# Kernel optimization log

Hardware: AMD Instinct MI355X
Metric: run time of the kernel (lower is better)

The kernel has to match this reference:

```python
import jax, jax.numpy as jnp
import numpy as np

B, H, N, HD = 8, 12, 577, 64   # batch, heads, tokens (576 patches + CLS), head dim
GRID = 24                      # 384 / 16
TEMP = 0.1                     # RelaxedBernoulli temperature
EPS = 1e-6


def _make_dists():
    # pairwise (row,col) offsets between patch grid positions, CLS row/col padded with 0
    r, c = np.indices((GRID, GRID))
    idx = np.stack([r.ravel(), c.ravel()], axis=-1).astype(np.float32)   # (576, 2)
    d = idx[:, None, :] - idx[None, :, :]                                # (576, 576, 2)
    d = np.pad(d, ((1, 0), (1, 0), (0, 0)))                              # (577, 577, 2)
    return jnp.asarray(d)


def setup_inputs() -> dict:
    key = jax.random.key(0)
    kq, k1, k2, ku = jax.random.split(key, 4)
    return {
        "query": jax.random.normal(kq, (B, H, N, HD), dtype=jnp.float32),
        "W1": jax.random.normal(k1, (HD, 64), dtype=jnp.float32) * 0.02,
        "b1": jnp.zeros((64,), dtype=jnp.float32),
        "W2": jax.random.normal(k2, (64, 3), dtype=jnp.float32) * 0.02,
        "b2": jnp.zeros((3,), dtype=jnp.float32),
        "u": jax.random.uniform(ku, (B, H, N, N), dtype=jnp.float32,
                                minval=EPS, maxval=1.0 - EPS),
        "dists": _make_dists(),
    }


def reference(query, W1, b1, W2, b2, u, dists):
    # sigma MLP: Linear -> gelu -> Linear  ->  (b,h,n,3)
    s = jax.nn.gelu(query @ W1 + b1, approximate=False) @ W2 + b2

    # per-token 2x2 covariance: [[sx^2, rho*sx*sy], [rho*sx*sy, sy^2]]
    sx = jax.nn.relu(s[..., 0]) + 1.0
    sy = jax.nn.relu(s[..., 1]) + 1.0
    rho = 0.99 * jnp.tanh(s[..., 2])
    sxx = sx * sx
    syy = sy * sy
    sxy = rho * sx * sy

    # closed-form 2x2 inverse
    det = sxx * syy - sxy * sxy
    inv00 = syy / det
    inv11 = sxx / det
    inv01 = -sxy / det

    # quadratic form d^T Sinv d without materializing (b,h,n,n,2,2)
    dx = dists[..., 0]   # (n, n)
    dy = dists[..., 1]
    w = -0.5 * (jnp.einsum('bhi,ij->bhij', inv00, dx * dx)
                + 2.0 * jnp.einsum('bhi,ij->bhij', inv01, dx * dy)
                + jnp.einsum('bhi,ij->bhij', inv11, dy * dy))

    kernel = jnp.exp(w)
    probs = kernel / jnp.max(kernel, axis=-1, keepdims=True)
    probs = jnp.clip(probs, EPS, 1.0 - EPS)

    # RelaxedBernoulli reparameterized sample with logistic noise from u
    logits = jnp.log(probs) - jnp.log1p(-probs)
    noise = jnp.log(u) - jnp.log1p(-u)
    mask = jax.nn.sigmoid((logits + noise) / TEMP)
    return mask
```

## Files before the change

### kernel.cpp

```cpp
#include <hip/hip_runtime.h>
#include <math.h>

#define BHN     55392
#define NTOK    577
#define HD      64
#define EPS_F   1e-6f
#define TOTAL_ELEMS 31961184
#define TOTAL_VEC   7990296

__global__ __launch_bounds__(256) void sigma_coef_kernel(
    const float* __restrict__ q,  const float* __restrict__ W1,
    const float* __restrict__ b1, const float* __restrict__ W2,
    const float* __restrict__ b2, float4* __restrict__ coef)
{
    const int tok = blockIdx.x * 256 + threadIdx.x;
    if (tok >= BHN) return;

    float h[HD];
    #pragma unroll
    for (int t = 0; t < HD; ++t) h[t] = 0.0f;

    const float4* w1_4 = (const float4*)W1;
    const float4* q4   = (const float4*)(q + (size_t)tok * HD);
    float4 qv = q4[0];
    #pragma unroll 1
    for (int kk = 0; kk < 16; ++kk) {
        const int kn = (kk < 15) ? (kk + 1) : 15;
        float4 qnext = q4[kn];
        float qk[4] = {qv.x, qv.y, qv.z, qv.w};
        #pragma unroll
        for (int d = 0; d < 4; ++d) {
            float qs = qk[d];
            const int base = (kk * 4 + d) * 16;
            #pragma unroll
            for (int t4 = 0; t4 < 16; ++t4) {
                float4 wv = w1_4[base + t4];
                h[4*t4+0] = fmaf(qs, wv.x, h[4*t4+0]);
                h[4*t4+1] = fmaf(qs, wv.y, h[4*t4+1]);
                h[4*t4+2] = fmaf(qs, wv.z, h[4*t4+2]);
                h[4*t4+3] = fmaf(qs, wv.w, h[4*t4+3]);
            }
        }
        qv = qnext;
    }

    float s0 = b2[0], s1 = b2[1], s2 = b2[2];
    #pragma unroll
    for (int t = 0; t < HD; ++t) {
        float x = h[t] + b1[t];
        float z = x * 0.70710678118654752f;
        float az = fabsf(z);
        float k = __builtin_amdgcn_rcpf(fmaf(0.3275911f, az, 1.0f));
        float poly = k * (0.254829592f + k * (-0.284496736f +
                     k * (1.421413741f + k * (-1.453152027f +
                     k * 1.061405429f))));
        float om = poly * __expf(-z * z);
        float erfz = copysignf(1.0f - om, z);
        float g = 0.5f * x * (1.0f + erfz);
        s0 = fmaf(g, W2[t*3 + 0], s0);
        s1 = fmaf(g, W2[t*3 + 1], s1);
        s2 = fmaf(g, W2[t*3 + 2], s2);
    }

    float sx = fmaxf(s0, 0.0f) + 1.0f;
    float sy = fmaxf(s1, 0.0f) + 1.0f;
    float ex = __expf(2.0f * s2);
    float rho = 0.99f * ((ex - 1.0f) * __builtin_amdgcn_rcpf(ex + 1.0f));
    float sxx = sx * sx, syy = sy * sy;
    float sxy = rho * sx * sy;
    float det = sxx * syy - sxy * sxy;
    float inv_det = 1.0f / det;

    float a = -0.5f * syy * inv_det;
    float b =  sxy * inv_det;
    float c = -0.5f * sxx * inv_det;

    int i = tok % NTOK;
    float pack;
    if (i == 0) { a = 0.0f; b = 0.0f; c = 0.0f; pack = 0.0f; }
    else {
        int ip = i - 1;
        int ri = ip / 24;
        int ci = ip - ri * 24;
        pack = (float)(ri * 32 + ci);
    }
    coef[tok] = make_float4(a, b, c, pack);
}

__global__ __launch_bounds__(256) void mask_kernel(
    const float4* __restrict__ u4, const float4* __restrict__ coef,
    float4* __restrict__ out4)
{
    int vid = blockIdx.x * 256 + threadIdx.x;
    if (vid >= TOTAL_VEC) return;

    int e0 = vid * 4;
    unsigned row0 = (unsigned)e0 / 577u;
    int j0 = e0 - (int)row0 * 577;

    unsigned row1 = row0 + ((j0 + 3 >= 577) ? 1u : 0u);
    float4 cf0 = coef[row0];
    float4 cf1 = coef[row1];
    float4 uu = u4[vid];

    float um[4] = {uu.x, uu.y, uu.z, uu.w};
    float res[4];

    #pragma unroll
    for (int m = 0; m < 4; ++m) {
        int j = j0 + m;
        bool crossed = (j >= 577);
        if (crossed) j -= 577;
        float4 cf;
        cf.x = crossed ? cf1.x : cf0.x;
        cf.y = crossed ? cf1.y : cf0.y;
        cf.z = crossed ? cf1.z : cf0.z;
        cf.w = crossed ? cf1.w : cf0.w;
        int rc = (int)cf.w;

        float dx = 0.0f, dy = 0.0f;
        if (j > 0) {
            unsigned jj = (unsigned)(j - 1);
            unsigned rj = jj / 24u;
            unsigned cj = jj - rj * 24u;
            dx = (float)((rc >> 5) - (int)rj);
            dy = (float)((rc & 31) - (int)cj);
        }

        float w = fmaf(fmaf(cf.x, dx, cf.y * dy), dx, cf.z * (dy * dy));

        float p = __expf(w);
        p = fminf(fmaxf(p, EPS_F), 1.0f - EPS_F);

        float uk  = um[m];
        float num = p * uk;
        float den = (1.0f - p) * (1.0f - uk);
        float r   = den * __builtin_amdgcn_rcpf(num);

        float r2  = r * r;
        float r4  = r2 * r2;
        float r5  = r4 * r;
        float r10 = r5 * r5;

        res[m] = __builtin_amdgcn_rcpf(1.0f + r10);
    }

    out4[vid] = make_float4(res[0], res[1], res[2], res[3]);
}

extern "C" void kernel_launch(void* const* d_in, const int* in_sizes, int n_in,
                              void* d_out, int out_size, void* d_ws, size_t ws_size,
                              hipStream_t stream) {
    const float* q  = (const float*)d_in[0];
    const float* W1 = (const float*)d_in[1];
    const float* b1 = (const float*)d_in[2];
    const float* W2 = (const float*)d_in[3];
    const float* b2 = (const float*)d_in[4];
    const float* u  = (const float*)d_in[5];

    float4* coef = (float4*)d_ws;

    sigma_coef_kernel<<<(BHN + 255) / 256, 256, 0, stream>>>(q, W1, b1, W2, b2, coef);
    mask_kernel<<<(TOTAL_VEC + 255) / 256, 256, 0, stream>>>(
        (const float4*)u, coef, (float4*)d_out);
}
```

Baseline: 266.6 us.

## Split sigma MLP hidden dimension across 8 lanes per token with shuffle reduction

The sigma MLP kernel now assigns 8 threads per token, each computing 8 of the 64 hidden units, and combines the three output partial sums with xor-shuffles. This cuts per-thread register use (64 accumulators down to 8) and launches 8x more threads, which should raise occupancy and parallelism for the small first kernel. In exchange, each lane reloads the full query row, the reduction adds shuffles, and only one lane in eight does the final covariance math and store. The mask kernel, which likely dominates the total time, is unchanged.

```diff
diff --git a/kernel.cpp b/kernel.cpp
--- a/kernel.cpp
+++ b/kernel.cpp
@@ -13,15 +13,19 @@
     const float* __restrict__ b1, const float* __restrict__ W2,
     const float* __restrict__ b2, float4* __restrict__ coef)
 {
-    const int tok = blockIdx.x * 256 + threadIdx.x;
+    const int tid   = threadIdx.x;
+    const int slice = tid & 7;
+    const int tok   = blockIdx.x * 32 + (tid >> 3);
     if (tok >= BHN) return;
 
-    float h[HD];
+    float h[8];
     #pragma unroll
-    for (int t = 0; t < HD; ++t) h[t] = 0.0f;
+    for (int t = 0; t < 8; ++t) h[t] = 0.0f;
 
-    const float4* w1_4 = (const float4*)W1;
-    const float4* q4   = (const float4*)(q + (size_t)tok * HD);
+    const float4* q4    = (const float4*)(q + (size_t)tok * HD);
+    const float4* w1_4  = (const float4*)W1;
+    const int     woff  = slice * 2;
+
     float4 qv = q4[0];
     #pragma unroll 1
     for (int kk = 0; kk < 16; ++kk) {
@@ -30,24 +34,27 @@
         float qk[4] = {qv.x, qv.y, qv.z, qv.w};
         #pragma unroll
         for (int d = 0; d < 4; ++d) {
+            const float4* wrow = w1_4 + (kk * 4 + d) * 16 + woff;
+            float4 w0 = wrow[0];
+            float4 w1v = wrow[1];
             float qs = qk[d];
-            const int base = (kk * 4 + d) * 16;
-            #pragma unroll
-            for (int t4 = 0; t4 < 16; ++t4) {
-                float4 wv = w1_4[base + t4];
-                h[4*t4+0] = fmaf(qs, wv.x, h[4*t4+0]);
-                h[4*t4+1] = fmaf(qs, wv.y, h[4*t4+1]);
-                h[4*t4+2] = fmaf(qs, wv.z, h[4*t4+2]);
-                h[4*t4+3] = fmaf(qs, wv.w, h[4*t4+3]);
-            }
+            h[0] = fmaf(qs, w0.x, h[0]);
+            h[1] = fmaf(qs, w0.y, h[1]);
+            h[2] = fmaf(qs, w0.z, h[2]);
+            h[3] = fmaf(qs, w0.w, h[3]);
+            h[4] = fmaf(qs, w1v.x, h[4]);
+            h[5] = fmaf(qs, w1v.y, h[5]);
+            h[6] = fmaf(qs, w1v.z, h[6]);
+            h[7] = fmaf(qs, w1v.w, h[7]);
         }
         qv = qnext;
     }
 
-    float s0 = b2[0], s1 = b2[1], s2 = b2[2];
+    float s0 = 0.0f, s1 = 0.0f, s2 = 0.0f;
+    const int tbase = slice * 8;
     #pragma unroll
-    for (int t = 0; t < HD; ++t) {
-        float x = h[t] + b1[t];
+    for (int t = 0; t < 8; ++t) {
+        float x = h[t] + b1[tbase + t];
         float z = x * 0.70710678118654752f;
         float az = fabsf(z);
         float k = __builtin_amdgcn_rcpf(fmaf(0.3275911f, az, 1.0f));
@@ -57,34 +64,41 @@
         float om = poly * __expf(-z * z);
         float erfz = copysignf(1.0f - om, z);
         float g = 0.5f * x * (1.0f + erfz);
-        s0 = fmaf(g, W2[t*3 + 0], s0);
-        s1 = fmaf(g, W2[t*3 + 1], s1);
-        s2 = fmaf(g, W2[t*3 + 2], s2);
+        s0 = fmaf(g, W2[(tbase + t)*3 + 0], s0);
+        s1 = fmaf(g, W2[(tbase + t)*3 + 1], s1);
+        s2 = fmaf(g, W2[(tbase + t)*3 + 2], s2);
     }
 
-    float sx = fmaxf(s0, 0.0f) + 1.0f;
-    float sy = fmaxf(s1, 0.0f) + 1.0f;
-    float ex = __expf(2.0f * s2);
-    float rho = 0.99f * ((ex - 1.0f) * __builtin_amdgcn_rcpf(ex + 1.0f));
-    float sxx = sx * sx, syy = sy * sy;
-    float sxy = rho * sx * sy;
-    float det = sxx * syy - sxy * sxy;
-    float inv_det = 1.0f / det;
+    s0 += __shfl_xor(s0, 1); s0 += __shfl_xor(s0, 2); s0 += __shfl_xor(s0, 4);
+    s1 += __shfl_xor(s1, 1); s1 += __shfl_xor(s1, 2); s1 += __shfl_xor(s1, 4);
+    s2 += __shfl_xor(s2, 1); s2 += __shfl_xor(s2, 2); s2 += __shfl_xor(s2, 4);
 
-    float a = -0.5f * syy * inv_det;
-    float b =  sxy * inv_det;
-    float c = -0.5f * sxx * inv_det;
+    if (slice == 0) {
+        s0 += b2[0]; s1 += b2[1]; s2 += b2[2];
+        float sx = fmaxf(s0, 0.0f) + 1.0f;
+        float sy = fmaxf(s1, 0.0f) + 1.0f;
+        float ex = __expf(2.0f * s2);
+        float rho = 0.99f * ((ex - 1.0f) * __builtin_amdgcn_rcpf(ex + 1.0f));
+        float sxx = sx * sx, syy = sy * sy;
+        float sxy = rho * sx * sy;
+        float det = sxx * syy - sxy * sxy;
+        float inv_det = 1.0f / det;
 
-    int i = tok % NTOK;
-    float pack;
-    if (i == 0) { a = 0.0f; b = 0.0f; c = 0.0f; pack = 0.0f; }
-    else {
-        int ip = i - 1;
-        int ri = ip / 24;
-        int ci = ip - ri * 24;
-        pack = (float)(ri * 32 + ci);
+        float a = -0.5f * syy * inv_det;
+        float b =  sxy * inv_det;
+        float c = -0.5f * sxx * inv_det;
+
+        int i = tok % NTOK;
+        float pack;
+        if (i == 0) { a = 0.0f; b = 0.0f; c = 0.0f; pack = 0.0f; }
+        else {
+            int ip = i - 1;
+            int ri = ip / 24;
+            int ci = ip - ri * 24;
+            pack = (float)(ri * 32 + ci);
+        }
+        coef[tok] = make_float4(a, b, c, pack);
     }
-    coef[tok] = make_float4(a, b, c, pack);
 }
 
 __global__ __launch_bounds__(256) void mask_kernel(
@@ -160,7 +174,7 @@
 
     float4* coef = (float4*)d_ws;
 
-    sigma_coef_kernel<<<(BHN + 255) / 256, 256, 0, stream>>>(q, W1, b1, W2, b2, coef);
+    sigma_coef_kernel<<<(BHN + 31) / 32, 256, 0, stream>>>(q, W1, b1, W2, b2, coef);
     mask_kernel<<<(TOTAL_VEC + 255) / 256, 256, 0, stream>>>(
         (const float4*)u, coef, (float4*)d_out);
 }
```

Measured after the change: 267.7 us. No clear change (+0.4%).

## Fuse sigma MLP into mask kernel with per-wave row MLP and nontemporal IO

Applied to the files above, without the earlier changes.

Merges the two launches into one kernel. Each block handles 4 rows: each wavefront computes one token's MLP with lanes over the hidden dimension and a shuffle reduction, then writes the coefficients to shared memory. The block then streams the 4 rows of u to output with nontemporal loads and stores. This removes the second launch and the coefficient round trip through global memory, at the cost of a per-block MLP phase and a barrier before streaming. It also leaves only about 577 vectors per 256-thread block, so some threads sit idle in the second loop iteration.

```diff
diff --git a/kernel.cpp b/kernel.cpp
--- a/kernel.cpp
+++ b/kernel.cpp
@@ -1,151 +1,139 @@
 #include <hip/hip_runtime.h>
 #include <math.h>
 
-#define BHN     55392
-#define NTOK    577
-#define HD      64
-#define EPS_F   1e-6f
-#define TOTAL_ELEMS 31961184
-#define TOTAL_VEC   7990296
+#define BHN    55392
+#define NTOK   577
+#define HD     64
+#define EPS_F  1e-6f
+#define ROWS_PER_BLOCK 4
+#define NBLOCKS (BHN / ROWS_PER_BLOCK)
+#define VEC_PER_BLOCK 577
 
-__global__ __launch_bounds__(256) void sigma_coef_kernel(
-    const float* __restrict__ q,  const float* __restrict__ W1,
-    const float* __restrict__ b1, const float* __restrict__ W2,
-    const float* __restrict__ b2, float4* __restrict__ coef)
+typedef float v4f __attribute__((ext_vector_type(4)));
+
+__global__ __launch_bounds__(256) void fused_mask_kernel(
+    const float*  __restrict__ q,  const float* __restrict__ W1,
+    const float*  __restrict__ b1, const float* __restrict__ W2,
+    const float*  __restrict__ b2, const v4f* __restrict__ u4,
+    v4f* __restrict__ out4)
 {
-    const int tok = blockIdx.x * 256 + threadIdx.x;
-    if (tok >= BHN) return;
+    __shared__ float4 coef_s[ROWS_PER_BLOCK];
 
-    float h[HD];
-    #pragma unroll
-    for (int t = 0; t < HD; ++t) h[t] = 0.0f;
+    const int tid  = threadIdx.x;
+    const int lane = tid & 63;
+    const int wv   = tid >> 6;
+    const int tok  = blockIdx.x * ROWS_PER_BLOCK + wv;
 
-    const float4* w1_4 = (const float4*)W1;
-    const float4* q4   = (const float4*)(q + (size_t)tok * HD);
-    float4 qv = q4[0];
-    #pragma unroll 1
-    for (int kk = 0; kk < 16; ++kk) {
-        const int kn = (kk < 15) ? (kk + 1) : 15;
-        float4 qnext = q4[kn];
-        float qk[4] = {qv.x, qv.y, qv.z, qv.w};
-        #pragma unroll
-        for (int d = 0; d < 4; ++d) {
-            float qs = qk[d];
-            const int base = (kk * 4 + d) * 16;
-            #pragma unroll
-            for (int t4 = 0; t4 < 16; ++t4) {
-                float4 wv = w1_4[base + t4];
-                h[4*t4+0] = fmaf(qs, wv.x, h[4*t4+0]);
-                h[4*t4+1] = fmaf(qs, wv.y, h[4*t4+1]);
-                h[4*t4+2] = fmaf(qs, wv.z, h[4*t4+2]);
-                h[4*t4+3] = fmaf(qs, wv.w, h[4*t4+3]);
-            }
-        }
-        qv = qnext;
-    }
+    {
+        const float* qrow = q + (size_t)tok * HD;
+        float h = 0.0f;
+        #pragma unroll 8
+        for (int k = 0; k < HD; ++k)
+            h = fmaf(qrow[k], W1[k * HD + lane], h);
 
-    float s0 = b2[0], s1 = b2[1], s2 = b2[2];
-    #pragma unroll
-    for (int t = 0; t < HD; ++t) {
-        float x = h[t] + b1[t];
-        float z = x * 0.70710678118654752f;
+        float x = h + b1[lane];
+        float z  = x * 0.70710678118654752f;
         float az = fabsf(z);
-        float k = __builtin_amdgcn_rcpf(fmaf(0.3275911f, az, 1.0f));
-        float poly = k * (0.254829592f + k * (-0.284496736f +
-                     k * (1.421413741f + k * (-1.453152027f +
-                     k * 1.061405429f))));
-        float om = poly * __expf(-z * z);
+        float kk = __builtin_amdgcn_rcpf(fmaf(0.3275911f, az, 1.0f));
+        float poly = kk * (0.254829592f + kk * (-0.284496736f +
+                     kk * (1.421413741f + kk * (-1.453152027f +
+                     kk * 1.061405429f))));
+        float om   = poly * __expf(-z * z);
         float erfz = copysignf(1.0f - om, z);
         float g = 0.5f * x * (1.0f + erfz);
-        s0 = fmaf(g, W2[t*3 + 0], s0);
-        s1 = fmaf(g, W2[t*3 + 1], s1);
-        s2 = fmaf(g, W2[t*3 + 2], s2);
-    }
 
-    float sx = fmaxf(s0, 0.0f) + 1.0f;
-    float sy = fmaxf(s1, 0.0f) + 1.0f;
-    float ex = __expf(2.0f * s2);
-    float rho = 0.99f * ((ex - 1.0f) * __builtin_amdgcn_rcpf(ex + 1.0f));
-    float sxx = sx * sx, syy = sy * sy;
-    float sxy = rho * sx * sy;
-    float det = sxx * syy - sxy * sxy;
-    float inv_det = 1.0f / det;
+        float s0 = g * W2[lane * 3 + 0];
+        float s1 = g * W2[lane * 3 + 1];
+        float s2 = g * W2[lane * 3 + 2];
 
-    float a = -0.5f * syy * inv_det;
-    float b =  sxy * inv_det;
-    float c = -0.5f * sxx * inv_det;
-
-    int i = tok % NTOK;
-    float pack;
-    if (i == 0) { a = 0.0f; b = 0.0f; c = 0.0f; pack = 0.0f; }
-    else {
-        int ip = i - 1;
-        int ri = ip / 24;
-        int ci = ip - ri * 24;
-        pack = (float)(ri * 32 + ci);
-    }
-    coef[tok] = make_float4(a, b, c, pack);
-}
-
-__global__ __launch_bounds__(256) void mask_kernel(
-    const float4* __restrict__ u4, const float4* __restrict__ coef,
-    float4* __restrict__ out4)
-{
-    int vid = blockIdx.x * 256 + threadIdx.x;
-    if (vid >= TOTAL_VEC) return;
-
-    int e0 = vid * 4;
-    unsigned row0 = (unsigned)e0 / 577u;
-    int j0 = e0 - (int)row0 * 577;
-
-    unsigned row1 = row0 + ((j0 + 3 >= 577) ? 1u : 0u);
-    float4 cf0 = coef[row0];
-    float4 cf1 = coef[row1];
-    float4 uu = u4[vid];
-
-    float um[4] = {uu.x, uu.y, uu.z, uu.w};
-    float res[4];
-
-    #pragma unroll
-    for (int m = 0; m < 4; ++m) {
-        int j = j0 + m;
-        bool crossed = (j >= 577);
-        if (crossed) j -= 577;
-        float4 cf;
-        cf.x = crossed ? cf1.x : cf0.x;
-        cf.y = crossed ? cf1.y : cf0.y;
-        cf.z = crossed ? cf1.z : cf0.z;
-        cf.w = crossed ? cf1.w : cf0.w;
-        int rc = (int)cf.w;
-
-        float dx = 0.0f, dy = 0.0f;
-        if (j > 0) {
-            unsigned jj = (unsigned)(j - 1);
-            unsigned rj = jj / 24u;
-            unsigned cj = jj - rj * 24u;
-            dx = (float)((rc >> 5) - (int)rj);
-            dy = (float)((rc & 31) - (int)cj);
+        #pragma unroll
+        for (int off = 1; off < 64; off <<= 1) {
+            s0 += __shfl_xor(s0, off);
+            s1 += __shfl_xor(s1, off);
+            s2 += __shfl_xor(s2, off);
         }
 
-        float w = fmaf(fmaf(cf.x, dx, cf.y * dy), dx, cf.z * (dy * dy));
+        if (lane == 0) {
+            s0 += b2[0]; s1 += b2[1]; s2 += b2[2];
+            float sx = fmaxf(s0, 0.0f) + 1.0f;
+            float sy = fmaxf(s1, 0.0f) + 1.0f;
+            float ex = __expf(2.0f * s2);
+            float rho = 0.99f * ((ex - 1.0f) * __builtin_amdgcn_rcpf(ex + 1.0f));
+            float sxx = sx * sx, syy = sy * sy;
+            float sxy = rho * sx * sy;
+            float det = sxx * syy - sxy * sxy;
+            float inv_det = 1.0f / det;
 
-        float p = __expf(w);
-        p = fminf(fmaxf(p, EPS_F), 1.0f - EPS_F);
+            float a = -0.5f * syy * inv_det;
+            float b =  sxy * inv_det;
+            float c = -0.5f * sxx * inv_det;
 
-        float uk  = um[m];
-        float num = p * uk;
-        float den = (1.0f - p) * (1.0f - uk);
-        float r   = den * __builtin_amdgcn_rcpf(num);
+            int i = tok % NTOK;
+            float pack;
+            if (i == 0) { a = 0.0f; b = 0.0f; c = 0.0f; pack = 0.0f; }
+            else {
+                int ip = i - 1;
+                int ri = ip / 24;
+                int ci = ip - ri * 24;
+                pack = (float)(ri * 32 + ci);
+            }
+            coef_s[wv] = make_float4(a, b, c, pack);
+        }
+    }
+    __syncthreads();
 
-        float r2  = r * r;
-        float r4  = r2 * r2;
-        float r5  = r4 * r;
-        float r10 = r5 * r5;
+    const float4 c0 = coef_s[0];
+    const float4 c1 = coef_s[1];
+    const float4 c2 = coef_s[2];
+    const float4 c3 = coef_s[3];
 
-        res[m] = __builtin_amdgcn_rcpf(1.0f + r10);
+    const size_t base = (size_t)blockIdx.x * VEC_PER_BLOCK;
+
+    #pragma unroll 1
+    for (int it = tid; it < VEC_PER_BLOCK; it += 256) {
+        v4f uu = __builtin_nontemporal_load(&u4[base + it]);
+        float um[4] = {uu.x, uu.y, uu.z, uu.w};
+        float res[4];
+
+        int e0 = it * 4;
+        #pragma unroll
+        for (int m = 0; m < 4; ++m) {
+            int e = e0 + m;
+            int rl = (e >= 1731) ? 3 : ((e >= 1154) ? 2 : ((e >= 577) ? 1 : 0));
+            int j  = e - rl * 577;
+            float4 cf = (rl == 0) ? c0 : ((rl == 1) ? c1 : ((rl == 2) ? c2 : c3));
+            int rc = (int)cf.w;
+
+            float dx = 0.0f, dy = 0.0f;
+            if (j > 0) {
+                unsigned jj = (unsigned)(j - 1);
+                unsigned rj = jj / 24u;
+                unsigned cj = jj - rj * 24u;
+                dx = (float)((rc >> 5) - (int)rj);
+                dy = (float)((rc & 31) - (int)cj);
+            }
+
+            float w = fmaf(fmaf(cf.x, dx, cf.y * dy), dx, cf.z * (dy * dy));
+
+            float p = __expf(w);
+            p = fminf(fmaxf(p, EPS_F), 1.0f - EPS_F);
+
+            float uk  = um[m];
+            float num = p * uk;
+            float den = (1.0f - p) * (1.0f - uk);
+            float r   = den * __builtin_amdgcn_rcpf(num);
+
+            float r2  = r * r;
+            float r4  = r2 * r2;
+            float r5  = r4 * r;
+            float r10 = r5 * r5;
+
+            res[m] = __builtin_amdgcn_rcpf(1.0f + r10);
+        }
+
+        v4f o = {res[0], res[1], res[2], res[3]};
+        __builtin_nontemporal_store(o, &out4[base + it]);
     }
-
-    out4[vid] = make_float4(res[0], res[1], res[2], res[3]);
 }
 
 extern "C" void kernel_launch(void* const* d_in, const int* in_sizes, int n_in,
@@ -158,9 +146,6 @@
     const float* b2 = (const float*)d_in[4];
     const float* u  = (const float*)d_in[5];
 
-    float4* coef = (float4*)d_ws;
-
-    sigma_coef_kernel<<<(BHN + 255) / 256, 256, 0, stream>>>(q, W1, b1, W2, b2, coef);
-    mask_kernel<<<(TOTAL_VEC + 255) / 256, 256, 0, stream>>>(
-        (const float4*)u, coef, (float4*)d_out);
+    fused_mask_kernel<<<NBLOCKS, 256, 0, stream>>>(
+        q, W1, b1, W2, b2, (const v4f*)u, (v4f*)d_out);
 }
```

After: 284.7 us. +6.8%, slower.
